# Performance work log

Hardware: AMD Instinct MI355X
Metric: run time of the kernel (lower is better)

## Reference

```python
import jax, jax.numpy as jnp
import numpy as np

NUM_BOXES = 16384
NUM_CLASS = 3
CODE_SIZE = 7
NMS_PRE = 1024
NMS_POST = 512
NMS_THRESH = 0.8
EPS = 1e-8


def _cross(a, b):
    return a[..., 0] * b[..., 1] - a[..., 1] * b[..., 0]


def _bev_corners(b5):
    # b5: (..., 5) = (cx, cy, dx, dy, ry) -> corners (..., 4, 2)
    c, s = jnp.cos(b5[..., 4]), jnp.sin(b5[..., 4])
    off = jnp.array([[0.5, 0.5], [-0.5, 0.5], [-0.5, -0.5], [0.5, -0.5]], dtype=b5.dtype)
    lx = b5[..., 2:3] * off[:, 0]  # (..., 4)
    ly = b5[..., 3:4] * off[:, 1]
    cx = b5[..., 0:1] + lx * c[..., None] - ly * s[..., None]
    cy = b5[..., 1:2] + lx * s[..., None] + ly * c[..., None]
    return jnp.stack([cx, cy], axis=-1)


def _points_in_box(p, b5):
    # p: (..., K, 2), b5: (..., 5) -> (..., K) bool (point inside rotated rect)
    c, s = jnp.cos(b5[..., 4:5]), jnp.sin(b5[..., 4:5])
    rel = p - b5[..., None, 0:2]
    qx = rel[..., 0] * c + rel[..., 1] * s
    qy = -rel[..., 0] * s + rel[..., 1] * c
    return (jnp.abs(qx) <= b5[..., 2:3] * 0.5 + 1e-5) & (jnp.abs(qy) <= b5[..., 3:4] * 0.5 + 1e-5)


def _pairwise_bev_iou(b5):
    # b5: (N, 5) -> (N, N) rotated BEV IoU (matches iou3d nms_gpu's BEV IoU)
    a = b5[:, None, :]
    b = b5[None, :, :]
    ca = _bev_corners(a)  # (N,1,4,2)
    cb = _bev_corners(b)  # (1,N,4,2)
    # edge-edge segment intersections: (N,N,4,4)
    a0, da = ca, jnp.roll(ca, -1, axis=-2) - ca
    b0, db = cb, jnp.roll(cb, -1, axis=-2) - cb
    A0, DA = a0[..., :, None, :], da[..., :, None, :]
    B0, DB = b0[..., None, :, :], db[..., None, :, :]
    den = _cross(DA, DB)
    d = B0 - A0
    den_s = jnp.where(jnp.abs(den) > EPS, den, 1.0)
    t = _cross(d, DB) / den_s
    u = _cross(d, DA) / den_s
    ok = (jnp.abs(den) > EPS) & (t >= 0) & (t <= 1) & (u >= 0) & (u <= 1)
    p_ee = A0 + t[..., None] * DA  # (N,N,4,4,2)
    shp = p_ee.shape[:-3]
    p_ee = p_ee.reshape(shp + (16, 2))
    ok = ok.reshape(shp + (16,))
    in_b = _points_in_box(ca, b)  # corners of A inside B: (N,N,4)
    in_a = _points_in_box(cb, a)  # corners of B inside A: (N,N,4)
    pts = jnp.concatenate([p_ee,
                           jnp.broadcast_to(ca, shp + (4, 2)),
                           jnp.broadcast_to(cb, shp + (4, 2))], axis=-2)  # (N,N,24,2)
    msk = jnp.concatenate([ok, in_b, in_a], axis=-1)  # (N,N,24)
    # order candidate vertices by angle around centroid (intersection is convex)
    cnt = jnp.maximum(msk.sum(-1, keepdims=True), 1)
    ctr = (pts * msk[..., None]).sum(-2, keepdims=True) / cnt[..., None]  # (N,N,1,2)
    ang = jnp.arctan2(pts[..., 1] - ctr[..., 1], pts[..., 0] - ctr[..., 0])
    ang = jnp.where(msk, ang, 1e9)  # invalid points sorted to the end
    order = jnp.argsort(ang, axis=-1)
    pts_s = jnp.take_along_axis(pts, order[..., None], axis=-2)
    msk_s = jnp.take_along_axis(msk, order, axis=-1)
    first = pts_s[..., 0:1, :]
    poly = jnp.where(msk_s[..., None], pts_s, first)  # pad with first vertex (zero shoelace contribution)
    inter = 0.5 * jnp.abs(_cross(poly, jnp.roll(poly, -1, axis=-2)).sum(-1))
    area_a = a[..., 2] * a[..., 3]
    area_b = b[..., 2] * b[..., 3]
    return inter / jnp.maximum(area_a + area_b - inter, 1e-6)


def _greedy_nms(iou, thresh):
    n = iou.shape[0]
    idx = jnp.arange(n)

    def body(i, supp):
        alive = jnp.logical_not(supp[i])
        return supp | (alive & (iou[i] > thresh) & (idx > i))

    supp = jax.lax.fori_loop(0, n, body, jnp.zeros((n,), dtype=bool))
    return ~supp


def _select_one(box_preds, cls_preds):
    # box_preds: (M, 7), cls_preds: (M, C) -> padded selected indices + validity
    scores = jnp.max(cls_preds, axis=1)
    _, top_idx = jax.lax.top_k(scores, NMS_PRE)  # score-descending, like torch.topk
    bev = box_preds[top_idx][:, jnp.array([0, 1, 3, 4, 6])]  # (cx,cy,dx,dy,ry)
    iou = _pairwise_bev_iou(bev)
    keep = _greedy_nms(iou, NMS_THRESH)
    pri = jnp.where(keep, jnp.arange(NMS_PRE), 2 * NMS_PRE)
    pos = jnp.sort(pri)[:NMS_POST]  # kept positions in score order
    valid = pos < NMS_PRE
    sel = top_idx[jnp.minimum(pos, NMS_PRE - 1)]
    return sel, valid


def setup_inputs() -> dict:
    key = jax.random.key(0)
    k1, k2, k3, k4, k5 = jax.random.split(key, 5)
    B = 2
    xy = jax.random.uniform(k1, (B, NUM_BOXES, 2), minval=-50.0, maxval=50.0)
    z = jax.random.uniform(k2, (B, NUM_BOXES, 1), minval=-2.0, maxval=1.0)
    dims = jax.random.uniform(k3, (B, NUM_BOXES, 3), minval=1.0, maxval=5.0)
    ry = jax.random.uniform(k4, (B, NUM_BOXES, 1), minval=-np.pi, maxval=np.pi)
    batch_box_preds = jnp.concatenate([xy, z, dims, ry], axis=-1).astype(jnp.float32)
    batch_cls_preds = (jax.random.normal(k5, (B, NUM_BOXES, NUM_CLASS)) * 3.0).astype(jnp.float32)
    return {"batch_box_preds": batch_box_preds, "batch_cls_preds": batch_cls_preds}


def reference(batch_box_preds, batch_cls_preds):
    # RoIHeadTemplate.proposal_layer: per-sample max-score, class-agnostic NMS,
    # scatter into zero-padded (B, NMS_POST, ...) tensors.
    sel, valid = jax.vmap(_select_one)(batch_box_preds, batch_cls_preds)  # (B, NMS_POST)
    rois = jnp.take_along_axis(batch_box_preds, sel[..., None], axis=1)
    logits = jnp.take_along_axis(batch_cls_preds, sel[..., None], axis=1)
    labels = jnp.argmax(logits, axis=-1)
    scores = jnp.max(logits, axis=-1)
    v = valid[..., None]
    rois = jnp.where(v, rois, 0.0)
    logits = jnp.where(v, logits, 0.0)
    scores = jnp.where(valid, scores, 0.0)
    roi_labels = jnp.where(valid, labels, 0) + 1  # padded slots end up as 1, same as torch (zeros + 1)
    return rois, scores, roi_labels, logits
```

## Files before the change

kernel.cpp:

```cpp
#include <hip/hip_runtime.h>
#include <hip/hip_bf16.h>
#include <math.h>

#define NBOX   16384
#define NPRE   1024
#define NPOST  512
#define NMS_TH 0.8f
#define DEN_EPS 1e-8f
#define NCAND  2048
#define NBUCK  8192

typedef unsigned long long ull;

__device__ __forceinline__ unsigned mono_f32(float a) {
  unsigned u = __float_as_uint(a);
  return (u & 0x80000000u) ? ~u : (u | 0x80000000u);
}

__global__ __launch_bounds__(1024) void k_hist(
    const float* __restrict__ cls, ull* __restrict__ cand,
    unsigned* __restrict__ candCount, unsigned* __restrict__ nz) {
  __shared__ unsigned hist[NBUCK];
  __shared__ unsigned wsuf[16];
  __shared__ unsigned thrT;
  __shared__ unsigned cnt;
  int b = blockIdx.x;
  int t = threadIdx.x;
  int lane = t & 63, wv = t >> 6;
  nz[b * NPRE + t] = 0u;
#pragma unroll
  for (int k = 0; k < NBUCK / 1024; ++k) hist[t + k * 1024] = 0u;
  if (t == 0) cnt = 0u;
  __syncthreads();

  ull key[16];
#pragma unroll
  for (int k = 0; k < 16; ++k) {
    int i = k * 1024 + t;
    const float* cc = cls + ((size_t)b * NBOX + i) * 3;
    float s = fmaxf(cc[0], fmaxf(cc[1], cc[2]));
    unsigned u = mono_f32(s);
    key[k] = ((ull)u << 14) | (ull)(16383 - i);
    atomicAdd(&hist[u >> 19], 1u);
  }
  __syncthreads();

  unsigned s8 = 0;
#pragma unroll
  for (int k = 0; k < 8; ++k) s8 += hist[t * 8 + k];
  unsigned v = s8;
#pragma unroll
  for (int off = 1; off < 64; off <<= 1) {
    unsigned o = __shfl_down(v, off, 64);
    if (lane + off < 64) v += o;
  }
  if (lane == 0) wsuf[wv] = v;
  __syncthreads();
  if (t < 16) {
    unsigned x = wsuf[t];
#pragma unroll
    for (int off = 1; off < 16; off <<= 1) {
      unsigned o = __shfl_down(x, off, 64);
      if (t + off < 16) x += o;
    }
    wsuf[t] = x;
  }
  __syncthreads();
  unsigned Sown = v + ((wv < 15) ? wsuf[wv + 1] : 0u);
  unsigned Snxt = Sown - s8;
  if (Sown >= NPRE && Snxt < NPRE) {
    unsigned c = Snxt;
    unsigned T = t * 8;
    for (int k = 7; k >= 0; --k) {
      c += hist[t * 8 + k];
      if (c >= NPRE) { T = t * 8 + k; break; }
    }
    thrT = T;
  }
  __syncthreads();
  unsigned T = thrT;
#pragma unroll
  for (int k = 0; k < 16; ++k) {
    bool c = (unsigned)(key[k] >> 33) >= T;
    ull bal = __ballot(c);
    if (bal) {
      unsigned base = 0;
      if (lane == 0) base = atomicAdd(&cnt, (unsigned)__popcll(bal));
      base = (unsigned)__shfl((int)base, 0, 64);
      if (c) {
        unsigned pos = base + (unsigned)__popcll(bal & ((1ull << lane) - 1ull));
        if (pos < NCAND) cand[(size_t)b * NCAND + pos] = key[k];
      }
    }
  }
  __syncthreads();
  if (t == 0) candCount[b] = (cnt < NCAND) ? cnt : NCAND;
}

__global__ __launch_bounds__(256) void k_ranksel(
    const float* __restrict__ box, const ull* __restrict__ cand,
    const unsigned* __restrict__ candCount,
    int* __restrict__ topi, float* __restrict__ binfo, float4* __restrict__ pinfo) {
  __shared__ ull lk[NCAND];
  int b = blockIdx.y;
  int tid = threadIdx.x;
  int j = blockIdx.x * 256 + tid;
  unsigned C = candCount[b];
#pragma unroll
  for (int k = 0; k < NCAND / 256; ++k) {
    int idx = k * 256 + tid;
    lk[idx] = ((unsigned)idx < C) ? cand[(size_t)b * NCAND + idx] : 0ULL;
  }
  __syncthreads();
  ull my = ((unsigned)j < C) ? lk[j] : 0ULL;
  int r = 0;
  const ulonglong2* p2 = (const ulonglong2*)lk;
#pragma unroll 8
  for (int k = 0; k < NCAND / 2; ++k) {
    ulonglong2 kk = p2[k];
    r += (kk.x > my) ? 1 : 0;
    r += (kk.y > my) ? 1 : 0;
  }
  if ((unsigned)j >= C || r >= NPRE) return;
  int i = 16383 - (int)(my & 0x3FFFULL);
  topi[b * NPRE + r] = i;
  const float* bp = box + ((size_t)b * NBOX + i) * 7;
  float x = bp[0], y = bp[1], dx = bp[3], dy = bp[4], ry = bp[6];
  float c = cosf(ry), s = sinf(ry);
  float* o = binfo + ((size_t)b * NPRE + r) * 16;
  o[0] = x; o[1] = y; o[2] = dx; o[3] = dy; o[4] = c; o[5] = s;
  const float offx[4] = {0.5f, -0.5f, -0.5f, 0.5f};
  const float offy[4] = {0.5f, 0.5f, -0.5f, -0.5f};
#pragma unroll
  for (int k = 0; k < 4; ++k) {
    float lx = dx * offx[k], ly = dy * offy[k];
    o[6 + k]  = x + lx * c - ly * s;
    o[10 + k] = y + lx * s + ly * c;
  }
  float rad = 0.5f * sqrtf(dx * dx + dy * dy);
  float area = dx * dy;
  o[14] = rad; o[15] = area;
  pinfo[(size_t)b * NPRE + r] = make_float4(x, y, rad, area);
}

__device__ bool iou_exact_gt(const float* __restrict__ Ab, const float* __restrict__ Bb) {
  float ax = Ab[0], ay = Ab[1], bx = Bb[0], by = Bb[1];
  float aA = Ab[15], aB = Bb[15];
  float acx[4], acy[4], bcx[4], bcy[4];
#pragma unroll
  for (int k = 0; k < 4; ++k) {
    acx[k] = Ab[6 + k]; acy[k] = Ab[10 + k];
    bcx[k] = Bb[6 + k]; bcy[k] = Bb[10 + k];
  }
  float px[24], py[24];
  bool act[24];
#pragma unroll
  for (int p = 0; p < 4; ++p) {
    float A0x = acx[p], A0y = acy[p];
    float DAx = acx[(p + 1) & 3] - A0x, DAy = acy[(p + 1) & 3] - A0y;
#pragma unroll
    for (int q = 0; q < 4; ++q) {
      float B0x = bcx[q], B0y = bcy[q];
      float DBx = bcx[(q + 1) & 3] - B0x, DBy = bcy[(q + 1) & 3] - B0y;
      float den = DAx * DBy - DAy * DBx;
      float dxx = B0x - A0x, dyy = B0y - A0y;
      bool dok = fabsf(den) > DEN_EPS;
      float dens = dok ? den : 1.0f;
      float t = (dxx * DBy - dyy * DBx) / dens;
      float u = (dxx * DAy - dyy * DAx) / dens;
      int k = p * 4 + q;
      px[k] = A0x + t * DAx;
      py[k] = A0y + t * DAy;
      act[k] = dok && t >= 0.f && t <= 1.f && u >= 0.f && u <= 1.f;
    }
  }
  float cA = Ab[4], sA = Ab[5], cB = Bb[4], sB = Bb[5];
#pragma unroll
  for (int k = 0; k < 4; ++k) {
    float rx = acx[k] - bx, ry = acy[k] - by;
    float qx =  rx * cB + ry * sB, qy = -rx * sB + ry * cB;
    px[16 + k] = acx[k]; py[16 + k] = acy[k];
    act[16 + k] = (fabsf(qx) <= Bb[2] * 0.5f + 1e-5f) && (fabsf(qy) <= Bb[3] * 0.5f + 1e-5f);
  }
#pragma unroll
  for (int k = 0; k < 4; ++k) {
    float rx = bcx[k] - ax, ry = bcy[k] - ay;
    float qx =  rx * cA + ry * sA, qy = -rx * sA + ry * cA;
    px[20 + k] = bcx[k]; py[20 + k] = bcy[k];
    act[20 + k] = (fabsf(qx) <= Ab[2] * 0.5f + 1e-5f) && (fabsf(qy) <= Ab[3] * 0.5f + 1e-5f);
  }
  int cnt = 0; float sx = 0.f, sy = 0.f;
#pragma unroll
  for (int k = 0; k < 24; ++k)
    if (act[k]) { cnt++; sx += px[k]; sy += py[k]; }
  float fc = (float)(cnt > 1 ? cnt : 1);
  float cx0 = sx / fc, cy0 = sy / fc;
  ull key[24];
#pragma unroll
  for (int k = 0; k < 24; ++k) {
    float ang = atan2f(py[k] - cy0, px[k] - cx0);
    key[k] = act[k] ? ((((ull)mono_f32(ang)) << 5) | (ull)k) : ~0ull;
  }
  ull kmin = ~0ull; float fx = 0.f, fy = 0.f;
#pragma unroll
  for (int k = 0; k < 24; ++k) {
    bool lt = key[k] < kmin;
    kmin = lt ? key[k] : kmin;
    fx = lt ? px[k] : fx;
    fy = lt ? py[k] : fy;
  }
  float ssum = 0.f;
#pragma unroll
  for (int k = 0; k < 24; ++k) {
    ull myk = key[k];
    ull best = ~0ull; float nx = fx, ny = fy;
#pragma unroll
    for (int j = 0; j < 24; ++j) {
      bool c = (key[j] > myk) && (key[j] < best);
      best = c ? key[j] : best;
      nx = c ? px[j] : nx;
      ny = c ? py[j] : ny;
    }
    float contrib = px[k] * ny - py[k] * nx;
    ssum += (myk != ~0ull) ? contrib : 0.f;
  }
  float inter = 0.5f * fabsf(ssum);
  float uni = aA + aB - inter;
  return inter / fmaxf(uni, 1e-6f) > NMS_TH;
}

__global__ __launch_bounds__(256) void k_pairs(
    const float* __restrict__ binfo, const float4* __restrict__ pinfo,
    ull* __restrict__ mask, unsigned* __restrict__ nz) {
  int wv = (blockIdx.x * 256 + threadIdx.x) >> 6;
  int lane = threadIdx.x & 63;
  int w = wv & 15;
  int i = (wv >> 4) & (NPRE - 1);
  int b = wv >> 14;
  if (w * 64 + 63 <= i) return;
  int j = w * 64 + lane;
  float4 pj = pinfo[(size_t)b * NPRE + j];
  float4 pi = pinfo[(size_t)b * NPRE + i];
  bool cand = false;
  if (j > i) {
    float ddx = pi.x - pj.x, ddy = pi.y - pj.y;
    float rr = pi.z + pj.z + 1e-3f;
    if (ddx * ddx + ddy * ddy <= rr * rr) {
      float mn = fminf(pi.w, pj.w), mx = fmaxf(pi.w, pj.w);
      if (mn > NMS_TH * mx) cand = true;
    }
  }
  const float* base = binfo + (size_t)b * NPRE * 16;
  bool pred = cand && iou_exact_gt(base + (size_t)i * 16, base + (size_t)j * 16);
  ull bal = __ballot(pred);
  if (lane == 0 && bal) {
    mask[((size_t)b * NPRE + i) * 16 + w] = bal;
    atomicOr(&nz[b * NPRE + i], 1u << w);
  }
}

__global__ __launch_bounds__(1024) void k_final(
    const float* __restrict__ box, const float* __restrict__ cls,
    const int* __restrict__ topi, const ull* __restrict__ mask,
    const unsigned* __restrict__ nz, float* __restrict__ out, int B) {
  __shared__ ull remv_sh[16];
  int b = blockIdx.x;
  int p = threadIdx.x;
  int lane = p & 63, wid = p >> 6;

  if (wid == 0) {
    ull rfr[16];
#pragma unroll
    for (int w = 0; w < 16; ++w) {
      unsigned vz = nz[b * NPRE + w * 64 + lane];
      rfr[w] = __ballot(vz != 0u);
    }
    ull remv = 0;
    for (int w = 0; w < 16; ++w) {
      ull bb = rfr[w];
      while (bb) {
        int ii = __ffsll(bb) - 1;
        bb &= bb - 1;
        int row = w * 64 + ii;
        ull rw = __shfl(remv, w, 64);
        if (!((rw >> ii) & 1ULL)) {
          unsigned nzi = nz[b * NPRE + row];
          ull m = 0;
          if (lane < 16 && ((nzi >> lane) & 1u))
            m = mask[((size_t)b * NPRE + row) * 16 + lane];
          remv |= m;
        }
      }
    }
    if (lane < 16) remv_sh[lane] = remv;
  }
  __syncthreads();

  ull rw = remv_sh[wid];
  int alive = ((rw >> lane) & 1ULL) ? 0 : 1;
  int v = alive;
#pragma unroll
  for (int off = 1; off < 64; off <<= 1) {
    int t = __shfl_up(v, off, 64);
    if (lane >= off) v += t;
  }
  __shared__ int wtot[16], woff[17];
  if (lane == 63) wtot[wid] = v;
  __syncthreads();
  if (p == 0) {
    int acc = 0;
    for (int t = 0; t < 16; ++t) { woff[t] = acc; acc += wtot[t]; }
    woff[16] = acc;
  }
  __syncthreads();
  int excl = v - alive + woff[wid];
  int total = woff[16];
  float* rois   = out;
  float* scores = out + (size_t)B * NPOST * 7;
  float* labels = scores + (size_t)B * NPOST;
  float* logits = labels + (size_t)B * NPOST;
  if (alive && excl < NPOST) {
    int s = excl;
    int orig = topi[b * NPRE + p];
    const float* bb = box + ((size_t)b * NBOX + orig) * 7;
    float* ro = rois + ((size_t)b * NPOST + s) * 7;
#pragma unroll
    for (int c = 0; c < 7; ++c) ro[c] = bb[c];
    const float* cc = cls + ((size_t)b * NBOX + orig) * 3;
    float l0 = cc[0], l1 = cc[1], l2 = cc[2];
    float m = fmaxf(l0, fmaxf(l1, l2));
    int lab = (l0 == m) ? 0 : ((l1 == m) ? 1 : 2);
    scores[b * NPOST + s] = m;
    labels[b * NPOST + s] = (float)(lab + 1);
    float* lg = logits + ((size_t)b * NPOST + s) * 3;
    lg[0] = l0; lg[1] = l1; lg[2] = l2;
  }
  if (p < NPOST && p >= total) {
    float* ro = rois + ((size_t)b * NPOST + p) * 7;
#pragma unroll
    for (int c = 0; c < 7; ++c) ro[c] = 0.f;
    scores[b * NPOST + p] = 0.f;
    labels[b * NPOST + p] = 1.f;
    float* lg = logits + ((size_t)b * NPOST + p) * 3;
    lg[0] = 0.f; lg[1] = 0.f; lg[2] = 0.f;
  }
}

extern "C" void kernel_launch(void* const* d_in, const int* in_sizes, int n_in,
                              void* d_out, int out_size, void* d_ws, size_t ws_size,
                              hipStream_t stream) {
  const float* box = (const float*)d_in[0];
  const float* cls = (const float*)d_in[1];
  float* out = (float*)d_out;
  int B = in_sizes[0] / (NBOX * 7);

  char* w = (char*)d_ws;
  size_t off = 0;
  ull* cand        = (ull*)(w + off);      off += (size_t)B * NCAND * sizeof(ull);
  unsigned* candCt = (unsigned*)(w + off); off += (size_t)B * sizeof(unsigned);
  int* topi        = (int*)(w + off);      off += (size_t)B * NPRE * sizeof(int);
  off = (off + 63) & ~(size_t)63;
  float* binfo     = (float*)(w + off);    off += (size_t)B * NPRE * 16 * sizeof(float);
  float4* pinfo    = (float4*)(w + off);   off += (size_t)B * NPRE * sizeof(float4);
  ull* mask        = (ull*)(w + off);      off += (size_t)B * NPRE * 16 * sizeof(ull);
  unsigned* nz     = (unsigned*)(w + off); off += (size_t)B * NPRE * sizeof(unsigned);
  (void)off; (void)ws_size; (void)out_size; (void)n_in;

  hipLaunchKernelGGL(k_hist,    dim3(B), dim3(1024), 0, stream, cls, cand, candCt, nz);
  hipLaunchKernelGGL(k_ranksel, dim3(NCAND / 256, B), dim3(256), 0, stream, box, cand, candCt, topi, binfo, pinfo);
  hipLaunchKernelGGL(k_pairs,   dim3(B * NPRE * 16 / 4), dim3(256), 0, stream, binfo, pinfo, mask, nz);
  hipLaunchKernelGGL(k_final,   dim3(B), dim3(1024), 0, stream, box, cls, topi, mask, nz, out, B);
}
```

Baseline: 157.7 us.

## Compact candidate box pairs into a worklist and run exact IoU densely

The pair kernel no longer computes the exact rotated IoU inside each wavefront. It only filters candidates and appends the surviving (b,i,j) triples to a global worklist through an atomic counter. A new kernel then runs the exact IoU test over that worklist with a grid-stride loop and sets mask bits with atomicOr. The aim is to cut wavefront divergence from sparse candidates, at the price of an extra launch, global atomics and worklist traffic, with a fallback for worklist overflow.

```diff
diff --git a/kernel.cpp b/kernel.cpp
--- a/kernel.cpp
+++ b/kernel.cpp
@@ -9,6 +9,7 @@
 #define DEN_EPS 1e-8f
 #define NCAND  2048
 #define NBUCK  8192
+#define WMAX   (1u << 20)
 
 typedef unsigned long long ull;
 
@@ -19,7 +20,8 @@
 
 __global__ __launch_bounds__(1024) void k_hist(
     const float* __restrict__ cls, ull* __restrict__ cand,
-    unsigned* __restrict__ candCount, unsigned* __restrict__ nz) {
+    unsigned* __restrict__ candCount, unsigned* __restrict__ nz,
+    unsigned* __restrict__ wcnt) {
   __shared__ unsigned hist[NBUCK];
   __shared__ unsigned wsuf[16];
   __shared__ unsigned thrT;
@@ -28,6 +30,7 @@
   int t = threadIdx.x;
   int lane = t & 63, wv = t >> 6;
   nz[b * NPRE + t] = 0u;
+  if (b == 0 && t == 0) wcnt[0] = 0u;
 #pragma unroll
   for (int k = 0; k < NBUCK / 1024; ++k) hist[t + k * 1024] = 0u;
   if (t == 0) cnt = 0u;
@@ -231,6 +234,7 @@
 
 __global__ __launch_bounds__(256) void k_pairs(
     const float* __restrict__ binfo, const float4* __restrict__ pinfo,
+    unsigned* __restrict__ wl, unsigned* __restrict__ wcnt, unsigned wcap,
     ull* __restrict__ mask, unsigned* __restrict__ nz) {
   int wv = (blockIdx.x * 256 + threadIdx.x) >> 6;
   int lane = threadIdx.x & 63;
@@ -250,12 +254,41 @@
       if (mn > NMS_TH * mx) cand = true;
     }
   }
-  const float* base = binfo + (size_t)b * NPRE * 16;
-  bool pred = cand && iou_exact_gt(base + (size_t)i * 16, base + (size_t)j * 16);
-  ull bal = __ballot(pred);
-  if (lane == 0 && bal) {
-    mask[((size_t)b * NPRE + i) * 16 + w] = bal;
-    atomicOr(&nz[b * NPRE + i], 1u << w);
+  ull bal = __ballot(cand);
+  if (!bal) return;
+  if (lane == 0) mask[((size_t)b * NPRE + i) * 16 + w] = 0ull;
+  unsigned baseOff = 0;
+  if (lane == 0) baseOff = atomicAdd(wcnt, (unsigned)__popcll(bal));
+  baseOff = (unsigned)__shfl((int)baseOff, 0, 64);
+  if (cand) {
+    unsigned off = baseOff + (unsigned)__popcll(bal & ((1ull << lane) - 1ull));
+    if (off < wcap) {
+      wl[off] = ((unsigned)b << 20) | ((unsigned)i << 10) | (unsigned)j;
+    } else {
+      const float* base = binfo + (size_t)b * NPRE * 16;
+      if (iou_exact_gt(base + (size_t)i * 16, base + (size_t)j * 16)) {
+        atomicOr(&mask[((size_t)b * NPRE + i) * 16 + w], 1ull << lane);
+        atomicOr(&nz[b * NPRE + i], 1u << w);
+      }
+    }
+  }
+}
+
+__global__ __launch_bounds__(256) void k_iou(
+    const float* __restrict__ binfo, const unsigned* __restrict__ wl,
+    const unsigned* __restrict__ wcnt, unsigned wcap,
+    ull* __restrict__ mask, unsigned* __restrict__ nz) {
+  unsigned n = wcnt[0];
+  if (n > wcap) n = wcap;
+  unsigned stride = gridDim.x * 256;
+  for (unsigned t = blockIdx.x * 256 + threadIdx.x; t < n; t += stride) {
+    unsigned pk = wl[t];
+    unsigned b = pk >> 20, i = (pk >> 10) & 1023, j = pk & 1023;
+    const float* base = binfo + (size_t)b * NPRE * 16;
+    if (iou_exact_gt(base + (size_t)i * 16, base + (size_t)j * 16)) {
+      atomicOr(&mask[((size_t)b * NPRE + i) * 16 + (j >> 6)], 1ull << (j & 63));
+      atomicOr(&nz[b * NPRE + i], 1u << (j >> 6));
+    }
   }
 }
 
@@ -364,10 +397,18 @@
   float4* pinfo    = (float4*)(w + off);   off += (size_t)B * NPRE * sizeof(float4);
   ull* mask        = (ull*)(w + off);      off += (size_t)B * NPRE * 16 * sizeof(ull);
   unsigned* nz     = (unsigned*)(w + off); off += (size_t)B * NPRE * sizeof(unsigned);
-  (void)off; (void)ws_size; (void)out_size; (void)n_in;
-
-  hipLaunchKernelGGL(k_hist,    dim3(B), dim3(1024), 0, stream, cls, cand, candCt, nz);
+  unsigned* wcnt   = (unsigned*)(w + off); off += 64;
+  unsigned* wl     = (unsigned*)(w + off);
+  unsigned wcap = 0;
+  if (ws_size > off) {
+    size_t rem = (ws_size - off) / sizeof(unsigned);
+    wcap = (rem < (size_t)WMAX) ? (unsigned)rem : WMAX;
+  }
+  (void)out_size; (void)n_in;
+
+  hipLaunchKernelGGL(k_hist,    dim3(B), dim3(1024), 0, stream, cls, cand, candCt, nz, wcnt);
   hipLaunchKernelGGL(k_ranksel, dim3(NCAND / 256, B), dim3(256), 0, stream, box, cand, candCt, topi, binfo, pinfo);
-  hipLaunchKernelGGL(k_pairs,   dim3(B * NPRE * 16 / 4), dim3(256), 0, stream, binfo, pinfo, mask, nz);
+  hipLaunchKernelGGL(k_pairs,   dim3(B * NPRE * 16 / 4), dim3(256), 0, stream, binfo, pinfo, wl, wcnt, wcap, mask, nz);
+  hipLaunchKernelGGL(k_iou,     dim3(128), dim3(256), 0, stream, binfo, wl, wcnt, wcap, mask, nz);
   hipLaunchKernelGGL(k_final,   dim3(B), dim3(1024), 0, stream, box, cls, topi, mask, nz, out, B);
 }
```

Measured after the change: 132.4 us. 16.1% less time.
